# Kernel tuning notes

Hardware: AMD Instinct MI355X
Metric: run time of the kernel (lower is better)

The kernel has to match this reference:

```python
import jax, jax.numpy as jnp
import numpy as np

B, S, E, H, T, K, F = 2, 2048, 768, 12, 128, 16, 3072
DH = E // H


def _ln(x, s, b, eps=1e-6):
    mu = jnp.mean(x, axis=-1, keepdims=True)
    var = jnp.mean(jnp.square(x - mu), axis=-1, keepdims=True)
    return (x - mu) * jax.lax.rsqrt(var + eps) * s + b


def _forward(h, mask, W_topo, b_topo, W_m1, b_m1, W_m2, b_m2, ln_t_s, ln_t_b,
             W_p1, b_p1, W_p2, b_p2, ln1_s, ln1_b, Wq, Wk, Wv, W_gate, b_gate,
             W_o, b_o, ln2_s, ln2_b, W_f1, b_f1, W_f2, b_f2):
    # ---- TopologicalFeatureExtractor (on pre-LN hidden_states) ----
    topo = h @ W_topo + b_topo                                   # [B,S,T]
    hn = h / (jnp.linalg.norm(h, axis=-1, keepdims=True) + 1e-8)
    dist = 1.0 - jnp.einsum('bsd,btd->bst', hn, hn)              # cosine distance [B,S,S]
    dist = jnp.where(jnp.eye(S, dtype=bool)[None], 1e9, dist)    # mask self
    idx = jnp.argsort(dist, axis=-1)[:, :, :K]                   # k-NN indices [B,S,K]
    nd = jnp.take_along_axis(dist, idx, axis=-1)                 # [B,S,K]
    nf = jax.vmap(lambda t, i: t[i])(topo, idx)                  # gather neighbors [B,S,K,T]
    wts = jax.nn.softmax(-nd, axis=-1)[..., None]
    combined = topo + (nf * wts).sum(axis=2)
    t = jax.nn.relu(combined @ W_m1 + b_m1) @ W_m2 + b_m2
    t = _ln(t, ln_t_s, ln_t_b)
    pf = jax.nn.relu(t @ W_p1 + b_p1) @ W_p2 + b_p2              # persistence features [B,S,T]
    # ---- TopologicalAttention (pre-LN residual block) ----
    x = _ln(h, ln1_s, ln1_b)
    q = (x @ Wq).reshape(B, S, H, DH)
    k = (x @ Wk).reshape(B, S, H, DH)
    v = (x @ Wv).reshape(B, S, H, DH)
    scores = jnp.einsum('bqhd,bkhd->bhqk', q, k) / jnp.sqrt(jnp.asarray(DH, jnp.float32))
    scores = jnp.where(mask[:, None, None, :] == 0, -10000.0, scores)
    probs = jax.nn.softmax(scores, axis=-1)
    ctx = jnp.einsum('bhqk,bkhd->bqhd', probs, v).reshape(B, S, E)
    gate = jax.nn.sigmoid(jnp.concatenate([ctx, pf], axis=-1) @ W_gate + b_gate)
    ctx = gate * ctx + (1.0 - gate) * x                          # x is attention's input (post-LN)
    h = h + (ctx @ W_o + b_o)
    # ---- FFN block ----
    y = _ln(h, ln2_s, ln2_b)
    y = jax.nn.gelu(y @ W_f1 + b_f1, approximate=True)
    return h + (y @ W_f2 + b_f2)


def setup_inputs() -> dict:
    key = jax.random.key(0)
    ks = jax.random.split(key, 16)
    w = lambda k, shp: (0.02 * jax.random.normal(k, shp)).astype(jnp.float32)
    z = lambda shp: jnp.zeros(shp, jnp.float32)
    o = lambda shp: jnp.ones(shp, jnp.float32)
    return {
        'hidden_states': jax.random.normal(ks[0], (B, S, E), jnp.float32),
        'attention_mask': jnp.ones((B, S), jnp.int32),
        'W_topo': w(ks[1], (E, T)), 'b_topo': z((T,)),
        'W_m1': w(ks[2], (T, 2 * T)), 'b_m1': z((2 * T,)),
        'W_m2': w(ks[3], (2 * T, T)), 'b_m2': z((T,)),
        'ln_t_s': o((T,)), 'ln_t_b': z((T,)),
        'W_p1': w(ks[4], (T, T)), 'b_p1': z((T,)),
        'W_p2': w(ks[5], (T, T)), 'b_p2': z((T,)),
        'ln1_s': o((E,)), 'ln1_b': z((E,)),
        'Wq': w(ks[6], (E, E)), 'Wk': w(ks[7], (E, E)), 'Wv': w(ks[8], (E, E)),
        'W_gate': w(ks[9], (E + T, E)), 'b_gate': z((E,)),
        'W_o': w(ks[10], (E, E)), 'b_o': z((E,)),
        'ln2_s': o((E,)), 'ln2_b': z((E,)),
        'W_f1': w(ks[11], (E, F)), 'b_f1': z((F,)),
        'W_f2': w(ks[12], (F, E)), 'b_f2': z((E,)),
    }


def reference(hidden_states, attention_mask, W_topo, b_topo, W_m1, b_m1, W_m2, b_m2,
              ln_t_s, ln_t_b, W_p1, b_p1, W_p2, b_p2, ln1_s, ln1_b, Wq, Wk, Wv,
              W_gate, b_gate, W_o, b_o, ln2_s, ln2_b, W_f1, b_f1, W_f2, b_f2):
    return _forward(hidden_states, attention_mask, W_topo, b_topo, W_m1, b_m1, W_m2, b_m2,
                    ln_t_s, ln_t_b, W_p1, b_p1, W_p2, b_p2, ln1_s, ln1_b, Wq, Wk, Wv,
                    W_gate, b_gate, W_o, b_o, ln2_s, ln2_b, W_f1, b_f1, W_f2, b_f2)
```

## Files before the change

kernel.cpp:

```cpp
#include <hip/hip_runtime.h>
#include <hip/hip_bf16.h>
#include <math.h>

#define BDIM 2
#define SDIM 2048
#define EDIM 768
#define HDIM 12
#define TDIM 128
#define KNN  16
#define FDIM 3072
#define DHD  64
#define BS   (BDIM*SDIM)

typedef __attribute__((ext_vector_type(8))) short short8;
typedef __attribute__((ext_vector_type(4))) float f32x4;
typedef __attribute__((ext_vector_type(2))) unsigned u32x2;

__device__ __forceinline__ short f2bf(float f) {
  unsigned u = __float_as_uint(f);
  u = u + 0x7fff + ((u >> 16) & 1);
  return (short)(u >> 16);
}
__device__ __forceinline__ float bf2f(short s) {
  return __uint_as_float(((unsigned)(unsigned short)s) << 16);
}
__device__ __forceinline__ unsigned cvt_pk_bf16(float a, float b) {
  unsigned r;
  asm("v_cvt_pk_bf16_f32 %0, %1, %2" : "=v"(r) : "v"(a), "v"(b));
  return r;
}
__device__ __forceinline__ float exp2_fast(float x) {
  float r;
  asm("v_exp_f32 %0, %1" : "=v"(r) : "v"(x));
  return r;
}
__device__ __forceinline__ void cp16(void* lds, const void* g) {
  __builtin_amdgcn_global_load_lds(
      (const __attribute__((address_space(1))) unsigned int*)g,
      (__attribute__((address_space(3))) unsigned int*)lds, 16, 0, 0);
}

__device__ __forceinline__ void block_reduce_sum2(float& a, float& b) {
  __shared__ float sa[4], sb[4];
  #pragma unroll
  for (int off = 32; off > 0; off >>= 1) {
    a += __shfl_xor(a, off);
    b += __shfl_xor(b, off);
  }
  int wid = threadIdx.x >> 6;
  if ((threadIdx.x & 63) == 0) { sa[wid] = a; sb[wid] = b; }
  __syncthreads();
  a = sa[0] + sa[1] + sa[2] + sa[3];
  b = sb[0] + sb[1] + sb[2] + sb[3];
}

struct WcSeg { const float* src; short* dst; int K, N, ntx, start; };
struct WcArgs { WcSeg s[8]; };

__global__ __launch_bounds__(256) void wconv_all(WcArgs a) {
  __shared__ float tile[64][65];
  const int bid = blockIdx.x;
  int si = 0;
  #pragma unroll
  for (int i = 1; i < 8; ++i) if (bid >= a.s[i].start) si = i;
  const float* W = a.s[si].src;
  short* Wt = a.s[si].dst;
  const int K = a.s[si].K, N = a.s[si].N;
  const int t = bid - a.s[si].start;
  const int n0 = (t % a.s[si].ntx)*64, k0 = (t / a.s[si].ntx)*64;
  const int tid = threadIdx.x;
  for (int i = tid; i < 4096; i += 256) {
    int r = i>>6, c = i&63;
    tile[r][c] = W[(size_t)(k0+r)*N + n0 + c];
  }
  __syncthreads();
  for (int i = tid; i < 4096; i += 256) {
    int r = i>>6, c = i&63;
    Wt[(size_t)(n0+r)*K + k0 + c] = f2bf(tile[c][r]);
  }
}

__global__ __launch_bounds__(256) void vtrans_kernel(
    const short* __restrict__ qkv, short* __restrict__ vt) {
  __shared__ short t[64][72];
  const int s0 = blockIdx.x*64;
  const int bh = blockIdx.y;
  const int b = bh / HDIM, h = bh % HDIM;
  const int tid = threadIdx.x;
  for (int i = tid; i < 512; i += 256) {
    int r = i>>3, c8 = (i&7)<<3;
    *(short8*)&t[r][c8] =
        *(const short8*)&qkv[(size_t)(b*SDIM+s0+r)*2304 + 1536 + h*DHD + c8];
  }
  __syncthreads();
  for (int i = tid; i < 512; i += 256) {
    int d = i>>3, c8 = (i&7)<<3;
    short8 pk;
    #pragma unroll
    for (int j = 0; j < 8; ++j) pk[j] = t[c8+j][d];
    *(short8*)&vt[(size_t)(bh*DHD+d)*SDIM + s0 + c8] = pk;
  }
}

__global__ __launch_bounds__(256) void norm_ln1_kernel(
    const float* __restrict__ h, const float* __restrict__ s,
    const float* __restrict__ bb, short* __restrict__ hb,
    short* __restrict__ hh, short* __restrict__ hl,
    float* __restrict__ x, short* __restrict__ xb) {
  int row = blockIdx.x;
  const float* hr = h + (size_t)row * EDIM;
  float v[3], s1 = 0.f, s2 = 0.f;
  #pragma unroll
  for (int t = 0; t < 3; ++t) {
    v[t] = hr[threadIdx.x + 256*t];
    s1 += v[t]; s2 += v[t]*v[t];
  }
  block_reduce_sum2(s1, s2);
  float mu  = s1 * (1.f/EDIM);
  float var = s2 * (1.f/EDIM) - mu*mu;
  float rs  = rsqrtf(var + 1e-6f);
  float invn = 1.f / (sqrtf(s2) + 1e-8f);
  #pragma unroll
  for (int t = 0; t < 3; ++t) {
    int i = threadIdx.x + 256*t;
    size_t idx = (size_t)row*EDIM + i;
    hb[idx] = f2bf(v[t]);
    float hnv = v[t]*invn;
    short hi = f2bf(hnv);
    hh[idx] = hi;
    hl[idx] = f2bf(hnv - bf2f(hi));
    float xv = (v[t]-mu)*rs*s[i] + bb[i];
    x[idx] = xv;
    xb[idx] = f2bf(xv);
  }
}

__global__ __launch_bounds__(256) void ln_bf_kernel(
    const float* __restrict__ in, const float* __restrict__ s,
    const float* __restrict__ bb, short* __restrict__ outb) {
  int row = blockIdx.x;
  const float* r = in + (size_t)row * EDIM;
  float v[3], s1 = 0.f, s2 = 0.f;
  #pragma unroll
  for (int t = 0; t < 3; ++t) {
    v[t] = r[threadIdx.x + 256*t];
    s1 += v[t]; s2 += v[t]*v[t];
  }
  block_reduce_sum2(s1, s2);
  float mu  = s1 * (1.f/EDIM);
  float var = s2 * (1.f/EDIM) - mu*mu;
  float rs  = rsqrtf(var + 1e-6f);
  #pragma unroll
  for (int t = 0; t < 3; ++t) {
    int i = threadIdx.x + 256*t;
    outb[(size_t)row*EDIM + i] = f2bf((v[t]-mu)*rs*s[i] + bb[i]);
  }
}

template<int ACT, int OUTBF>
__global__ __launch_bounds__(256) void gemm_mfma(
    const short* __restrict__ A, const short* __restrict__ Wt,
    const float* __restrict__ bias, const float* res,
    float* Cf, short* Cb, int Cb_ld,
    const float* __restrict__ blc, const float* __restrict__ blx,
    int K, int N) {
  __shared__ __align__(16) short As[128*64];
  __shared__ __align__(16) short Bs[128*64];
  const int bm = blockIdx.y*128, bn = blockIdx.x*128;
  const int tid = threadIdx.x;
  const int w = tid>>6, lane = tid&63, l15 = lane&15, g = lane>>4;
  const int wm = (w>>1)*64, wn = (w&1)*64;
  f32x4 acc[4][4] = {};
  for (int k0 = 0; k0 < K; k0 += 64) {
    #pragma unroll
    for (int it = 0; it < 4; ++it) {
      int p = (it*256 + tid)*16;
      int row = p >> 7;
      int slot = (p >> 4) & 7;
      int ss = slot ^ (row & 7);
      cp16((char*)As + it*4096 + w*1024, A  + (size_t)(bm+row)*K + k0 + ss*8);
      cp16((char*)Bs + it*4096 + w*1024, Wt + (size_t)(bn+row)*K + k0 + ss*8);
    }
    __syncthreads();
    #pragma unroll
    for (int ks = 0; ks < 2; ++ks) {
      short8 af[4], bfv[4];
      #pragma unroll
      for (int mt = 0; mt < 4; ++mt) {
        int r = wm + mt*16 + l15;
        af[mt] = *(const short8*)&As[r*64 + (((ks*4+g) ^ (r&7))*8)];
      }
      #pragma unroll
      for (int nt = 0; nt < 4; ++nt) {
        int r = wn + nt*16 + l15;
        bfv[nt] = *(const short8*)&Bs[r*64 + (((ks*4+g) ^ (r&7))*8)];
      }
      #pragma unroll
      for (int mt = 0; mt < 4; ++mt)
        #pragma unroll
        for (int nt = 0; nt < 4; ++nt)
          acc[mt][nt] = __builtin_amdgcn_mfma_f32_16x16x32_bf16(af[mt], bfv[nt], acc[mt][nt], 0, 0, 0);
    }
    __syncthreads();
  }
  #pragma unroll
  for (int mt = 0; mt < 4; ++mt) {
    #pragma unroll
    for (int nt = 0; nt < 4; ++nt) {
      #pragma unroll
      for (int reg = 0; reg < 4; ++reg) {
        int row = bm + wm + mt*16 + g*4 + reg;
        int col = bn + wn + nt*16 + l15;
        float v = acc[mt][nt][reg];
        if (bias) v += bias[col];
        if (ACT == 2) {
          float xx = v;
          float t2 = 0.7978845608028654f*(xx + 0.044715f*xx*xx*xx);
          v = 0.5f*xx*(1.f + tanhf(t2));
        }
        if (ACT == 3) {
          float gg = 1.f/(1.f + expf(-v));
          size_t ix = (size_t)row*EDIM + col;
          float mv = gg*blc[ix] + (1.f-gg)*blx[ix];
          Cb[(size_t)row*Cb_ld + col] = f2bf(mv);
        } else {
          if (res) v += res[(size_t)row*N + col];
          if (OUTBF) Cb[(size_t)row*Cb_ld + col] = f2bf(v);
          else       Cf[(size_t)row*N + col] = v;
        }
      }
    }
  }
}

__global__ __launch_bounds__(256) void dist_mfma(
    const short* __restrict__ Hh, const short* __restrict__ Hl,
    float* __restrict__ dist) {
  __shared__ __align__(16) short Ah[128*64], Al[128*64];
  __shared__ __align__(16) short Bh[128*64], Bl[128*64];
  const int bm = blockIdx.y*128, bn = blockIdx.x*128;
  const int tid = threadIdx.x;
  const int w = tid>>6, lane = tid&63, l15 = lane&15, g = lane>>4;
  const int wm = (w>>1)*64, wn = (w&1)*64;
  f32x4 acc[4][4] = {};
  for (int k0 = 0; k0 < EDIM; k0 += 64) {
    #pragma unroll
    for (int it = 0; it < 4; ++it) {
      int p = (it*256 + tid)*16;
      int row = p >> 7;
      int slot = (p >> 4) & 7;
      int ss = slot ^ (row & 7);
      size_t ga = (size_t)(bm+row)*EDIM + k0 + ss*8;
      size_t gb = (size_t)(bn+row)*EDIM + k0 + ss*8;
      cp16((char*)Ah + it*4096 + w*1024, Hh + ga);
      cp16((char*)Al + it*4096 + w*1024, Hl + ga);
      cp16((char*)Bh + it*4096 + w*1024, Hh + gb);
      cp16((char*)Bl + it*4096 + w*1024, Hl + gb);
    }
    __syncthreads();
    #pragma unroll
    for (int ks = 0; ks < 2; ++ks) {
      short8 ah[4], al[4], bh[4], bl[4];
      #pragma unroll
      for (int mt = 0; mt < 4; ++mt) {
        int r = wm + mt*16 + l15;
        int o = r*64 + (((ks*4+g) ^ (r&7))*8);
        ah[mt] = *(const short8*)&Ah[o];
        al[mt] = *(const short8*)&Al[o];
      }
      #pragma unroll
      for (int nt = 0; nt < 4; ++nt) {
        int r = wn + nt*16 + l15;
        int o = r*64 + (((ks*4+g) ^ (r&7))*8);
        bh[nt] = *(const short8*)&Bh[o];
        bl[nt] = *(const short8*)&Bl[o];
      }
      #pragma unroll
      for (int mt = 0; mt < 4; ++mt)
        #pragma unroll
        for (int nt = 0; nt < 4; ++nt) {
          acc[mt][nt] = __builtin_amdgcn_mfma_f32_16x16x32_bf16(ah[mt], bh[nt], acc[mt][nt], 0, 0, 0);
          acc[mt][nt] = __builtin_amdgcn_mfma_f32_16x16x32_bf16(ah[mt], bl[nt], acc[mt][nt], 0, 0, 0);
          acc[mt][nt] = __builtin_amdgcn_mfma_f32_16x16x32_bf16(al[mt], bh[nt], acc[mt][nt], 0, 0, 0);
        }
    }
    __syncthreads();
  }
  #pragma unroll
  for (int mt = 0; mt < 4; ++mt) {
    #pragma unroll
    for (int nt = 0; nt < 4; ++nt) {
      #pragma unroll
      for (int reg = 0; reg < 4; ++reg) {
        int row = bm + wm + mt*16 + g*4 + reg;
        int col = bn + wn + nt*16 + l15;
        float v = 1.f - acc[mt][nt][reg];
        if (row == col) v = 1e9f;
        dist[(size_t)row*SDIM + col] = v;
      }
    }
  }
}

__global__ __launch_bounds__(256) void topk_kernel(
    const float* __restrict__ dist, const float* __restrict__ topob,
    float* __restrict__ combb) {
  int s = blockIdx.x;
  __shared__ float wbv[4];
  __shared__ int   wbi[4];
  __shared__ float nd[KNN];
  __shared__ int   nidx[KNN];
  __shared__ float wts[KNN];
  const int tid = threadIdx.x, lane = tid & 63, wid = tid >> 6;
  const float* drow = dist + (size_t)s*SDIM;
  float lv[8];
  float best = 3e38f; int bidx = 1<<30;
  #pragma unroll
  for (int j = 0; j < 8; ++j) {
    int i = tid + j*256;
    float v = drow[i];
    lv[j] = v;
    if (v < best) { best = v; bidx = i; }
  }
  for (int pass = 0; pass < KNN; ++pass) {
    float bv = best; int bi = bidx;
    #pragma unroll
    for (int off = 32; off > 0; off >>= 1) {
      float ov = __shfl_xor(bv, off);
      int   oi = __shfl_xor(bi, off);
      if (ov < bv || (ov == bv && oi < bi)) { bv = ov; bi = oi; }
    }
    if (lane == 0) { wbv[wid] = bv; wbi[wid] = bi; }
    __syncthreads();
    if (tid == 0) {
      float fv = wbv[0]; int fi = wbi[0];
      #pragma unroll
      for (int q2 = 1; q2 < 4; ++q2)
        if (wbv[q2] < fv || (wbv[q2] == fv && wbi[q2] < fi)) { fv = wbv[q2]; fi = wbi[q2]; }
      nd[pass] = fv; nidx[pass] = fi;
    }
    __syncthreads();
    int wi = nidx[pass];
    if ((wi & 255) == tid) {
      int jj = wi >> 8;
      #pragma unroll
      for (int j = 0; j < 8; ++j) if (j == jj) lv[j] = 3e38f;
      best = 3e38f; bidx = 1<<30;
      #pragma unroll
      for (int j = 0; j < 8; ++j)
        if (lv[j] < best) { best = lv[j]; bidx = tid + j*256; }
    }
    __syncthreads();
  }
  if (tid == 0) {
    float m = -nd[0];
    for (int k2 = 1; k2 < KNN; ++k2) m = fmaxf(m, -nd[k2]);
    float ssum = 0.f;
    for (int k2 = 0; k2 < KNN; ++k2) { float e = expf(-nd[k2] - m); wts[k2] = e; ssum += e; }
    float inv = 1.f/ssum;
    for (int k2 = 0; k2 < KNN; ++k2) wts[k2] *= inv;
  }
  __syncthreads();
  if (tid < TDIM) {
    float acc = topob[(size_t)s*TDIM + tid];
    #pragma unroll
    for (int k2 = 0; k2 < KNN; ++k2) acc += wts[k2]*topob[(size_t)nidx[k2]*TDIM + tid];
    combb[(size_t)s*TDIM + tid] = acc;
  }
}

__global__ __launch_bounds__(256) void topo_mlp_kernel(
    const float* __restrict__ comb,
    const float* __restrict__ W1, const float* __restrict__ b1,
    const float* __restrict__ W2, const float* __restrict__ b2,
    const float* __restrict__ lns, const float* __restrict__ lnb,
    const float* __restrict__ Wp1, const float* __restrict__ bp1,
    const float* __restrict__ Wp2, const float* __restrict__ bp2,
    short* __restrict__ cat) {
  int row = blockIdx.x;
  __shared__ float c[TDIM], a1[2*TDIM], t2[TDIM];
  __shared__ float red[8];
  const int tid = threadIdx.x;
  if (tid < TDIM) c[tid] = comb[(size_t)row*TDIM + tid];
  __syncthreads();
  {
    float a = b1[tid];
    for (int i = 0; i < TDIM; ++i) a += c[i]*W1[i*2*TDIM + tid];
    a1[tid] = fmaxf(a, 0.f);
  }
  __syncthreads();
  float tval = 0.f;
  if (tid < TDIM) {
    float a = b2[tid];
    for (int i = 0; i < 2*TDIM; ++i) a += a1[i]*W2[i*TDIM + tid];
    tval = a;
  }
  float s1 = (tid < TDIM) ? tval : 0.f;
  float s2 = (tid < TDIM) ? tval*tval : 0.f;
  #pragma unroll
  for (int off = 32; off > 0; off >>= 1) { s1 += __shfl_xor(s1, off); s2 += __shfl_xor(s2, off); }
  if ((tid & 63) == 0) { red[tid>>6] = s1; red[4 + (tid>>6)] = s2; }
  __syncthreads();
  s1 = red[0]+red[1]+red[2]+red[3];
  s2 = red[4]+red[5]+red[6]+red[7];
  float mu  = s1 * (1.f/TDIM);
  float var = s2 * (1.f/TDIM) - mu*mu;
  float rs  = rsqrtf(var + 1e-6f);
  if (tid < TDIM) t2[tid] = (tval - mu)*rs*lns[tid] + lnb[tid];
  __syncthreads();
  if (tid < TDIM) {
    float a = bp1[tid];
    for (int i = 0; i < TDIM; ++i) a += t2[i]*Wp1[i*TDIM + tid];
    a1[tid] = fmaxf(a, 0.f);
  }
  __syncthreads();
  if (tid < TDIM) {
    float a = bp2[tid];
    for (int i = 0; i < TDIM; ++i) a += a1[i]*Wp2[i*TDIM + tid];
    cat[(size_t)row*896 + 768 + tid] = f2bf(a);
  }
}

__global__ __launch_bounds__(256) void attn_mfma(
    const short* __restrict__ qkv, const short* __restrict__ vtb,
    const int* __restrict__ maskp,
    float* __restrict__ ctx, short* __restrict__ ctxb) {
  __shared__ __align__(16) short Ks[128*64];
  __shared__ __align__(16) short Vs[64*128];
  __shared__ __align__(16) short Ps[4*16*128];
  __shared__ float Ms[128];
  const float SCL = 0.18033688011112042f;
  const float MASKVAL = -14426.950408889634f;
  const int qb0 = blockIdx.x*64;
  const int hh = blockIdx.y, b = blockIdx.z;
  const int bh = b*HDIM + hh;
  const int tid = threadIdx.x;
  const int w = tid>>6, lane = tid&63, l15 = lane&15, g = lane>>4;
  short8 qf[2];
  {
    size_t rbase = (size_t)(b*SDIM + qb0 + w*16 + l15)*2304 + hh*DHD;
    qf[0] = *(const short8*)&qkv[rbase + g*8];
    qf[1] = *(const short8*)&qkv[rbase + 32 + g*8];
  }
  f32x4 acc[4] = {};
  float m_run = -1e30f, l_run = 0.f;
  char* PsW = (char*)Ps + w*4096 + l15*256;
  const int swz = (l15 & 7) << 1;
  for (int kt = 0; kt < SDIM; kt += 128) {
    #pragma unroll
    for (int it = 0; it < 4; ++it) {
      int t = it*256 + tid;
      int row = t>>3, slot = t&7, ss = slot ^ (row&7);
      cp16((char*)Ks + it*4096 + w*1024,
           qkv + (size_t)(b*SDIM+kt+row)*2304 + 768 + hh*DHD + ss*8);
    }
    #pragma unroll
    for (int it = 0; it < 4; ++it) {
      int t = it*256 + tid;
      int row = t>>4, slot = t&15, ss = slot ^ (row&15);
      cp16((char*)Vs + it*4096 + w*1024,
           vtb + (size_t)(bh*DHD+row)*SDIM + kt + ss*8);
    }
    if (tid < 128) Ms[tid] = (float)maskp[b*SDIM + kt + tid];
    __syncthreads();
    f32x4 s[8] = {};
    #pragma unroll
    for (int ks = 0; ks < 2; ++ks) {
      #pragma unroll
      for (int ct = 0; ct < 8; ++ct) {
        int r = ct*16 + l15;
        short8 kb8 = *(const short8*)&Ks[r*64 + (((ks*4+g) ^ (r&7))*8)];
        s[ct] = __builtin_amdgcn_mfma_f32_16x16x32_bf16(kb8, qf[ks], s[ct], 0, 0, 0);
      }
    }
    float rm = -1e30f;
    #pragma unroll
    for (int ct = 0; ct < 8; ++ct) {
      float4 mk = *(const float4*)&Ms[ct*16 + g*4];
      float v0 = s[ct][0]*SCL; if (mk.x == 0.f) v0 = MASKVAL;
      float v1 = s[ct][1]*SCL; if (mk.y == 0.f) v1 = MASKVAL;
      float v2 = s[ct][2]*SCL; if (mk.z == 0.f) v2 = MASKVAL;
      float v3 = s[ct][3]*SCL; if (mk.w == 0.f) v3 = MASKVAL;
      s[ct][0] = v0; s[ct][1] = v1; s[ct][2] = v2; s[ct][3] = v3;
      rm = fmaxf(rm, fmaxf(fmaxf(v0, v1), fmaxf(v2, v3)));
    }
    rm = fmaxf(rm, __shfl_xor(rm, 16));
    rm = fmaxf(rm, __shfl_xor(rm, 32));
    if (__any(rm > m_run + 11.5415603f)) {
      float mnew = fmaxf(m_run, rm);
      float corr = exp2_fast(m_run - mnew);
      l_run *= corr;
      #pragma unroll
      for (int reg = 0; reg < 4; ++reg) {
        float cq = __shfl(corr, (g<<4) | (g*4 + reg));
        #pragma unroll
        for (int dt = 0; dt < 4; ++dt) acc[dt][reg] *= cq;
      }
      m_run = mnew;
    }
    float rs = 0.f;
    #pragma unroll
    for (int ct = 0; ct < 8; ++ct) {
      float p0 = exp2_fast(s[ct][0] - m_run);
      float p1 = exp2_fast(s[ct][1] - m_run);
      float p2 = exp2_fast(s[ct][2] - m_run);
      float p3 = exp2_fast(s[ct][3] - m_run);
      rs += (p0 + p1) + (p2 + p3);
      u32x2 pk;
      pk.x = cvt_pk_bf16(p0, p1);
      pk.y = cvt_pk_bf16(p2, p3);
      int slot = ct*4 + g;
      *(u32x2*)(PsW + ((slot ^ swz) << 3)) = pk;
    }
    rs += __shfl_xor(rs, 16);
    rs += __shfl_xor(rs, 32);
    l_run += rs;
    #pragma unroll
    for (int ks2 = 0; ks2 < 4; ++ks2) {
      int s0 = ks2*8 + g*2;
      short8 pa = *(const short8*)(PsW + ((s0 ^ swz) << 3));
      #pragma unroll
      for (int dt = 0; dt < 4; ++dt) {
        int r = dt*16 + l15;
        short8 vb8 = *(const short8*)&Vs[r*128 + (((ks2*4+g) ^ (r&15))*8)];
        acc[dt] = __builtin_amdgcn_mfma_f32_16x16x32_bf16(pa, vb8, acc[dt], 0, 0, 0);
      }
    }
    __syncthreads();
  }
  float invq[4];
  #pragma unroll
  for (int reg = 0; reg < 4; ++reg)
    invq[reg] = 1.f / __shfl(l_run, (g<<4) | (g*4 + reg));
  #pragma unroll
  for (int dt = 0; dt < 4; ++dt) {
    #pragma unroll
    for (int reg = 0; reg < 4; ++reg) {
      int row = b*SDIM + qb0 + w*16 + g*4 + reg;
      float v = acc[dt][reg]*invq[reg];
      ctx [(size_t)row*EDIM + hh*DHD + dt*16 + l15] = v;
      ctxb[(size_t)row*896  + hh*DHD + dt*16 + l15] = f2bf(v);
    }
  }
}

extern "C" void kernel_launch(void* const* d_in, const int* in_sizes, int n_in,
                              void* d_out, int out_size, void* d_ws, size_t ws_size,
                              hipStream_t stream) {
  const float* h      = (const float*)d_in[0];
  const int*   mask   = (const int*)  d_in[1];
  const float* W_topo = (const float*)d_in[2];
  const float* b_topo = (const float*)d_in[3];
  const float* W_m1   = (const float*)d_in[4];
  const float* b_m1   = (const float*)d_in[5];
  const float* W_m2   = (const float*)d_in[6];
  const float* b_m2   = (const float*)d_in[7];
  const float* ln_t_s = (const float*)d_in[8];
  const float* ln_t_b = (const float*)d_in[9];
  const float* W_p1   = (const float*)d_in[10];
  const float* b_p1   = (const float*)d_in[11];
  const float* W_p2   = (const float*)d_in[12];
  const float* b_p2   = (const float*)d_in[13];
  const float* ln1_s  = (const float*)d_in[14];
  const float* ln1_b  = (const float*)d_in[15];
  const float* Wq     = (const float*)d_in[16];
  const float* Wk     = (const float*)d_in[17];
  const float* Wv     = (const float*)d_in[18];
  const float* W_gate = (const float*)d_in[19];
  const float* b_gate = (const float*)d_in[20];
  const float* W_o    = (const float*)d_in[21];
  const float* b_o    = (const float*)d_in[22];
  const float* ln2_s  = (const float*)d_in[23];
  const float* ln2_b  = (const float*)d_in[24];
  const float* W_f1   = (const float*)d_in[25];
  const float* b_f1   = (const float*)d_in[26];
  const float* W_f2   = (const float*)d_in[27];
  const float* b_f2   = (const float*)d_in[28];
  float* out = (float*)d_out;

  const size_t R = (size_t)BS*EDIM;
  short* wt_topo = (short*)d_ws;
  short* wt_qkv  = wt_topo + (size_t)128*768;
  short* wt_g    = wt_qkv  + (size_t)2304*768;
  short* wt_o    = wt_g    + (size_t)768*896;
  short* wt_f1   = wt_o    + (size_t)768*768;
  short* wt_f2   = wt_f1   + (size_t)3072*768;
  short* regA    = wt_f2   + (size_t)768*3072;
  short* regBCE  = regA + R;
  short* regD    = regBCE + 3*R;
  short* cat     = regD + R;
  float* xf      = (float*)(cat + (size_t)BS*896);
  float* Ff      = xf + R;
  short* vtb     = (short*)(Ff + (size_t)SDIM*SDIM);

  short* h_bf  = regA;
  short* mixb  = regA;
  short* hn_hi = regBCE;
  short* hn_lo = regBCE + R;
  float* topo  = (float*)(regBCE + 2*R);
  float* comb  = topo + (size_t)BS*TDIM;
  short* qkvb  = regBCE;
  short* x_bf  = regD;
  short* y_bf  = regD;
  float* dbuf  = Ff;
  float* ctxf  = Ff;
  short* ybuf  = (short*)Ff;

  WcArgs wa;
  wa.s[0] = {W_topo, wt_topo,                    EDIM, TDIM,  TDIM/64, 0};
  wa.s[1] = {Wq,     wt_qkv,                     EDIM, EDIM,  EDIM/64, 24};
  wa.s[2] = {Wk,     wt_qkv + (size_t)768*768,   EDIM, EDIM,  EDIM/64, 168};
  wa.s[3] = {Wv,     wt_qkv + (size_t)1536*768,  EDIM, EDIM,  EDIM/64, 312};
  wa.s[4] = {W_gate, wt_g,                       896,  EDIM,  EDIM/64, 456};
  wa.s[5] = {W_o,    wt_o,                       EDIM, EDIM,  EDIM/64, 624};
  wa.s[6] = {W_f1,   wt_f1,                      EDIM, FDIM,  FDIM/64, 768};
  wa.s[7] = {W_f2,   wt_f2,                      FDIM, EDIM,  EDIM/64, 1344};
  wconv_all<<<1920, 256, 0, stream>>>(wa);
  norm_ln1_kernel<<<BS, 256, 0, stream>>>(h, ln1_s, ln1_b, h_bf, hn_hi, hn_lo, xf, x_bf);
  gemm_mfma<0,0><<<dim3(1, BS/128), 256, 0, stream>>>(
      h_bf, wt_topo, b_topo, nullptr, topo, nullptr, 0, nullptr, nullptr, EDIM, TDIM);
  for (int b = 0; b < BDIM; ++b) {
    dist_mfma<<<dim3(SDIM/128, SDIM/128), 256, 0, stream>>>(
        hn_hi + (size_t)b*SDIM*EDIM, hn_lo + (size_t)b*SDIM*EDIM, dbuf);
    topk_kernel<<<SDIM, 256, 0, stream>>>(
        dbuf, topo + (size_t)b*SDIM*TDIM, comb + (size_t)b*SDIM*TDIM);
  }
  topo_mlp_kernel<<<BS, 256, 0, stream>>>(comb, W_m1, b_m1, W_m2, b_m2,
                                          ln_t_s, ln_t_b, W_p1, b_p1, W_p2, b_p2, cat);
  gemm_mfma<0,1><<<dim3(2304/128, BS/128), 256, 0, stream>>>(
      x_bf, wt_qkv, nullptr, nullptr, nullptr, qkvb, 2304, nullptr, nullptr, EDIM, 2304);
  vtrans_kernel<<<dim3(SDIM/64, BDIM*HDIM), 256, 0, stream>>>(qkvb, vtb);
  attn_mfma<<<dim3(SDIM/64, HDIM, BDIM), 256, 0, stream>>>(qkvb, vtb, mask, ctxf, cat);
  gemm_mfma<3,1><<<dim3(EDIM/128, BS/128), 256, 0, stream>>>(
      cat, wt_g, b_gate, nullptr, nullptr, mixb, EDIM, ctxf, xf, 896, EDIM);
  gemm_mfma<0,0><<<dim3(EDIM/128, BS/128), 256, 0, stream>>>(
      mixb, wt_o, b_o, h, out, nullptr, 0, nullptr, nullptr, EDIM, EDIM);
  ln_bf_kernel<<<BS, 256, 0, stream>>>(out, ln2_s, ln2_b, y_bf);
  gemm_mfma<2,1><<<dim3(FDIM/128, BS/128), 256, 0, stream>>>(
      y_bf, wt_f1, b_f1, nullptr, nullptr, ybuf, FDIM, nullptr, nullptr, EDIM, FDIM);
  gemm_mfma<0,0><<<dim3(EDIM/128, BS/128), 256, 0, stream>>>(
      ybuf, wt_f2, b_f2, out, out, nullptr, 0, nullptr, nullptr, FDIM, EDIM);
}
```

Before: 688.5 us.

## Double-buffer LDS tiles in GEMM and distance MFMA kernels

Both MFMA tile loops now use two LDS buffers. The tile for step k+1 is loaded while step k is computed, and one of the two barriers per K-step is removed. The aim is to hide global-to-LDS load latency behind the MFMA work. In exchange, LDS use per block doubles: 64KB for the GEMM and 128KB for the hi/lo distance kernel. That can lower the number of resident blocks per CU.

```diff
diff --git a/kernel.cpp b/kernel.cpp
--- a/kernel.cpp
+++ b/kernel.cpp
@@ -164,36 +164,43 @@
     float* Cf, short* Cb, int Cb_ld,
     const float* __restrict__ blc, const float* __restrict__ blx,
     int K, int N) {
-  __shared__ __align__(16) short As[128*64];
-  __shared__ __align__(16) short Bs[128*64];
+  __shared__ __align__(16) short As[2][128*64];
+  __shared__ __align__(16) short Bs[2][128*64];
   const int bm = blockIdx.y*128, bn = blockIdx.x*128;
   const int tid = threadIdx.x;
   const int w = tid>>6, lane = tid&63, l15 = lane&15, g = lane>>4;
   const int wm = (w>>1)*64, wn = (w&1)*64;
   f32x4 acc[4][4] = {};
-  for (int k0 = 0; k0 < K; k0 += 64) {
+
+  auto stage = [&](int buf, int k0) {
     #pragma unroll
     for (int it = 0; it < 4; ++it) {
       int p = (it*256 + tid)*16;
       int row = p >> 7;
-      int slot = (p >> 4) & 7;
-      int ss = slot ^ (row & 7);
-      cp16((char*)As + it*4096 + w*1024, A  + (size_t)(bm+row)*K + k0 + ss*8);
-      cp16((char*)Bs + it*4096 + w*1024, Wt + (size_t)(bn+row)*K + k0 + ss*8);
-    }
-    __syncthreads();
+      int ss = ((p >> 4) & 7) ^ (row & 7);
+      cp16((char*)&As[buf][0] + it*4096 + w*1024, A  + (size_t)(bm+row)*K + k0 + ss*8);
+      cp16((char*)&Bs[buf][0] + it*4096 + w*1024, Wt + (size_t)(bn+row)*K + k0 + ss*8);
+    }
+  };
+
+  const int nk = K >> 6;
+  stage(0, 0);
+  __syncthreads();
+  for (int t = 0; t < nk; ++t) {
+    const int cur = t & 1;
+    if (t + 1 < nk) stage(cur ^ 1, (t+1) << 6);
     #pragma unroll
     for (int ks = 0; ks < 2; ++ks) {
       short8 af[4], bfv[4];
       #pragma unroll
       for (int mt = 0; mt < 4; ++mt) {
         int r = wm + mt*16 + l15;
-        af[mt] = *(const short8*)&As[r*64 + (((ks*4+g) ^ (r&7))*8)];
+        af[mt] = *(const short8*)&As[cur][r*64 + (((ks*4+g) ^ (r&7))*8)];
       }
       #pragma unroll
       for (int nt = 0; nt < 4; ++nt) {
         int r = wn + nt*16 + l15;
-        bfv[nt] = *(const short8*)&Bs[r*64 + (((ks*4+g) ^ (r&7))*8)];
+        bfv[nt] = *(const short8*)&Bs[cur][r*64 + (((ks*4+g) ^ (r&7))*8)];
       }
       #pragma unroll
       for (int mt = 0; mt < 4; ++mt)
@@ -236,28 +243,35 @@
 __global__ __launch_bounds__(256) void dist_mfma(
     const short* __restrict__ Hh, const short* __restrict__ Hl,
     float* __restrict__ dist) {
-  __shared__ __align__(16) short Ah[128*64], Al[128*64];
-  __shared__ __align__(16) short Bh[128*64], Bl[128*64];
+  __shared__ __align__(16) short Ah[2][128*64], Al[2][128*64];
+  __shared__ __align__(16) short Bh[2][128*64], Bl[2][128*64];
   const int bm = blockIdx.y*128, bn = blockIdx.x*128;
   const int tid = threadIdx.x;
   const int w = tid>>6, lane = tid&63, l15 = lane&15, g = lane>>4;
   const int wm = (w>>1)*64, wn = (w&1)*64;
   f32x4 acc[4][4] = {};
-  for (int k0 = 0; k0 < EDIM; k0 += 64) {
+
+  auto stage = [&](int buf, int k0) {
     #pragma unroll
     for (int it = 0; it < 4; ++it) {
       int p = (it*256 + tid)*16;
       int row = p >> 7;
-      int slot = (p >> 4) & 7;
-      int ss = slot ^ (row & 7);
+      int ss = ((p >> 4) & 7) ^ (row & 7);
       size_t ga = (size_t)(bm+row)*EDIM + k0 + ss*8;
       size_t gb = (size_t)(bn+row)*EDIM + k0 + ss*8;
-      cp16((char*)Ah + it*4096 + w*1024, Hh + ga);
-      cp16((char*)Al + it*4096 + w*1024, Hl + ga);
-      cp16((char*)Bh + it*4096 + w*1024, Hh + gb);
-      cp16((char*)Bl + it*4096 + w*1024, Hl + gb);
-    }
-    __syncthreads();
+      cp16((char*)&Ah[buf][0] + it*4096 + w*1024, Hh + ga);
+      cp16((char*)&Al[buf][0] + it*4096 + w*1024, Hl + ga);
+      cp16((char*)&Bh[buf][0] + it*4096 + w*1024, Hh + gb);
+      cp16((char*)&Bl[buf][0] + it*4096 + w*1024, Hl + gb);
+    }
+  };
+
+  const int nk = EDIM >> 6;
+  stage(0, 0);
+  __syncthreads();
+  for (int t = 0; t < nk; ++t) {
+    const int cur = t & 1;
+    if (t + 1 < nk) stage(cur ^ 1, (t+1) << 6);
     #pragma unroll
     for (int ks = 0; ks < 2; ++ks) {
       short8 ah[4], al[4], bh[4], bl[4];
@@ -265,15 +279,15 @@
       for (int mt = 0; mt < 4; ++mt) {
         int r = wm + mt*16 + l15;
         int o = r*64 + (((ks*4+g) ^ (r&7))*8);
-        ah[mt] = *(const short8*)&Ah[o];
-        al[mt] = *(const short8*)&Al[o];
+        ah[mt] = *(const short8*)&Ah[cur][o];
+        al[mt] = *(const short8*)&Al[cur][o];
       }
       #pragma unroll
       for (int nt = 0; nt < 4; ++nt) {
         int r = wn + nt*16 + l15;
         int o = r*64 + (((ks*4+g) ^ (r&7))*8);
-        bh[nt] = *(const short8*)&Bh[o];
-        bl[nt] = *(const short8*)&Bl[o];
+        bh[nt] = *(const short8*)&Bh[cur][o];
+        bl[nt] = *(const short8*)&Bl[cur][o];
       }
       #pragma unroll
       for (int mt = 0; mt < 4; ++mt)
```

After: 761.3 us. 1.11x slower.

## Add N-tile template to GEMM and swizzle workgroup order across XCDs

Applied to the files above, without the earlier changes.

Makes the GEMM's N tile a template parameter and uses 64-wide tiles for the small-N GEMMs (topo, gate, W_o, FFN2), which doubles the workgroup count so more compute units on the chip get work. It also remaps block IDs in the GEMM and distance kernels so that consecutive blocks group by XCD, aiming for better L2 reuse. The narrower tiles give less reuse per block and run fewer MFMAs per A-tile load.

```diff
diff --git a/kernel.cpp b/kernel.cpp
--- a/kernel.cpp
+++ b/kernel.cpp
@@ -157,48 +157,59 @@
   }
 }
 
-template<int ACT, int OUTBF>
+template<int ACT, int OUTBF, int BN>
 __global__ __launch_bounds__(256) void gemm_mfma(
     const short* __restrict__ A, const short* __restrict__ Wt,
     const float* __restrict__ bias, const float* res,
     float* Cf, short* Cb, int Cb_ld,
     const float* __restrict__ blc, const float* __restrict__ blx,
     int K, int N) {
+  constexpr int NT = BN/32;
+  constexpr int BITER = BN/32;
   __shared__ __align__(16) short As[128*64];
-  __shared__ __align__(16) short Bs[128*64];
-  const int bm = blockIdx.y*128, bn = blockIdx.x*128;
+  __shared__ __align__(16) short Bs[BN*64];
+  const int nwg = gridDim.x * gridDim.y;
+  int bid = blockIdx.y * gridDim.x + blockIdx.x;
+  bid = (bid & 7) * (nwg >> 3) + (bid >> 3);
+  const int bm = (bid / gridDim.x) * 128;
+  const int bn = (bid % gridDim.x) * BN;
   const int tid = threadIdx.x;
   const int w = tid>>6, lane = tid&63, l15 = lane&15, g = lane>>4;
-  const int wm = (w>>1)*64, wn = (w&1)*64;
-  f32x4 acc[4][4] = {};
+  const int wm = (w>>1)*64, wn = (w&1)*(BN/2);
+  f32x4 acc[4][NT] = {};
   for (int k0 = 0; k0 < K; k0 += 64) {
     #pragma unroll
     for (int it = 0; it < 4; ++it) {
       int p = (it*256 + tid)*16;
       int row = p >> 7;
-      int slot = (p >> 4) & 7;
-      int ss = slot ^ (row & 7);
-      cp16((char*)As + it*4096 + w*1024, A  + (size_t)(bm+row)*K + k0 + ss*8);
+      int ss = ((p >> 4) & 7) ^ (row & 7);
+      cp16((char*)As + it*4096 + w*1024, A + (size_t)(bm+row)*K + k0 + ss*8);
+    }
+    #pragma unroll
+    for (int it = 0; it < BITER; ++it) {
+      int p = (it*256 + tid)*16;
+      int row = p >> 7;
+      int ss = ((p >> 4) & 7) ^ (row & 7);
       cp16((char*)Bs + it*4096 + w*1024, Wt + (size_t)(bn+row)*K + k0 + ss*8);
     }
     __syncthreads();
     #pragma unroll
     for (int ks = 0; ks < 2; ++ks) {
-      short8 af[4], bfv[4];
+      short8 af[4], bfv[NT];
       #pragma unroll
       for (int mt = 0; mt < 4; ++mt) {
         int r = wm + mt*16 + l15;
         af[mt] = *(const short8*)&As[r*64 + (((ks*4+g) ^ (r&7))*8)];
       }
       #pragma unroll
-      for (int nt = 0; nt < 4; ++nt) {
+      for (int nt = 0; nt < NT; ++nt) {
         int r = wn + nt*16 + l15;
         bfv[nt] = *(const short8*)&Bs[r*64 + (((ks*4+g) ^ (r&7))*8)];
       }
       #pragma unroll
       for (int mt = 0; mt < 4; ++mt)
         #pragma unroll
-        for (int nt = 0; nt < 4; ++nt)
+        for (int nt = 0; nt < NT; ++nt)
           acc[mt][nt] = __builtin_amdgcn_mfma_f32_16x16x32_bf16(af[mt], bfv[nt], acc[mt][nt], 0, 0, 0);
     }
     __syncthreads();
@@ -206,7 +217,7 @@
   #pragma unroll
   for (int mt = 0; mt < 4; ++mt) {
     #pragma unroll
-    for (int nt = 0; nt < 4; ++nt) {
+    for (int nt = 0; nt < NT; ++nt) {
       #pragma unroll
       for (int reg = 0; reg < 4; ++reg) {
         int row = bm + wm + mt*16 + g*4 + reg;
@@ -238,7 +249,11 @@
     float* __restrict__ dist) {
   __shared__ __align__(16) short Ah[128*64], Al[128*64];
   __shared__ __align__(16) short Bh[128*64], Bl[128*64];
-  const int bm = blockIdx.y*128, bn = blockIdx.x*128;
+  const int nwg = gridDim.x * gridDim.y;
+  int bid = blockIdx.y * gridDim.x + blockIdx.x;
+  bid = (bid & 7) * (nwg >> 3) + (bid >> 3);
+  const int bm = (bid / gridDim.x) * 128;
+  const int bn = (bid % gridDim.x) * 128;
   const int tid = threadIdx.x;
   const int w = tid>>6, lane = tid&63, l15 = lane&15, g = lane>>4;
   const int wm = (w>>1)*64, wn = (w&1)*64;
@@ -248,8 +263,7 @@
     for (int it = 0; it < 4; ++it) {
       int p = (it*256 + tid)*16;
       int row = p >> 7;
-      int slot = (p >> 4) & 7;
-      int ss = slot ^ (row & 7);
+      int ss = ((p >> 4) & 7) ^ (row & 7);
       size_t ga = (size_t)(bm+row)*EDIM + k0 + ss*8;
       size_t gb = (size_t)(bn+row)*EDIM + k0 + ss*8;
       cp16((char*)Ah + it*4096 + w*1024, Hh + ga);
@@ -617,7 +631,7 @@
   wa.s[7] = {W_f2,   wt_f2,                      FDIM, EDIM,  EDIM/64, 1344};
   wconv_all<<<1920, 256, 0, stream>>>(wa);
   norm_ln1_kernel<<<BS, 256, 0, stream>>>(h, ln1_s, ln1_b, h_bf, hn_hi, hn_lo, xf, x_bf);
-  gemm_mfma<0,0><<<dim3(1, BS/128), 256, 0, stream>>>(
+  gemm_mfma<0,0,64><<<dim3(TDIM/64, BS/128), 256, 0, stream>>>(
       h_bf, wt_topo, b_topo, nullptr, topo, nullptr, 0, nullptr, nullptr, EDIM, TDIM);
   for (int b = 0; b < BDIM; ++b) {
     dist_mfma<<<dim3(SDIM/128, SDIM/128), 256, 0, stream>>>(
@@ -627,17 +641,17 @@
   }
   topo_mlp_kernel<<<BS, 256, 0, stream>>>(comb, W_m1, b_m1, W_m2, b_m2,
                                           ln_t_s, ln_t_b, W_p1, b_p1, W_p2, b_p2, cat);
-  gemm_mfma<0,1><<<dim3(2304/128, BS/128), 256, 0, stream>>>(
+  gemm_mfma<0,1,128><<<dim3(2304/128, BS/128), 256, 0, stream>>>(
       x_bf, wt_qkv, nullptr, nullptr, nullptr, qkvb, 2304, nullptr, nullptr, EDIM, 2304);
   vtrans_kernel<<<dim3(SDIM/64, BDIM*HDIM), 256, 0, stream>>>(qkvb, vtb);
   attn_mfma<<<dim3(SDIM/64, HDIM, BDIM), 256, 0, stream>>>(qkvb, vtb, mask, ctxf, cat);
-  gemm_mfma<3,1><<<dim3(EDIM/128, BS/128), 256, 0, stream>>>(
+  gemm_mfma<3,1,64><<<dim3(EDIM/64, BS/128), 256, 0, stream>>>(
       cat, wt_g, b_gate, nullptr, nullptr, mixb, EDIM, ctxf, xf, 896, EDIM);
-  gemm_mfma<0,0><<<dim3(EDIM/128, BS/128), 256, 0, stream>>>(
+  gemm_mfma<0,0,64><<<dim3(EDIM/64, BS/128), 256, 0, stream>>>(
       mixb, wt_o, b_o, h, out, nullptr, 0, nullptr, nullptr, EDIM, EDIM);
   ln_bf_kernel<<<BS, 256, 0, stream>>>(out, ln2_s, ln2_b, y_bf);
-  gemm_mfma<2,1><<<dim3(FDIM/128, BS/128), 256, 0, stream>>>(
+  gemm_mfma<2,1,128><<<dim3(FDIM/128, BS/128), 256, 0, stream>>>(
       y_bf, wt_f1, b_f1, nullptr, nullptr, ybuf, FDIM, nullptr, nullptr, EDIM, FDIM);
-  gemm_mfma<0,0><<<dim3(EDIM/128, BS/128), 256, 0, stream>>>(
+  gemm_mfma<0,0,64><<<dim3(EDIM/64, BS/128), 256, 0, stream>>>(
       ybuf, wt_f2, b_f2, out, out, nullptr, 0, nullptr, nullptr, FDIM, EDIM);
 }
```

Measured after the change: 623.9 us. 9.4% less time.
